# Kernel tuning notes

Hardware: AMD Instinct MI355X
Metric: run time of the kernel (lower is better)

The kernel has to match this reference:

```python
import jax, jax.numpy as jnp
import numpy as np

N_EMBD = 1024
N_FF = 4 * N_EMBD
N_EXPERTS = 8
TOP_K = 2
B, S = 1, 2048


def setup_inputs() -> dict:
    key = jax.random.key(0)
    ks = jax.random.split(key, 8)
    std = 0.02
    x = jax.random.normal(ks[0], (B, S, N_EMBD), dtype=jnp.float32)
    Wr = jax.random.normal(ks[1], (N_EMBD, N_EXPERTS), dtype=jnp.float32) * std
    br = jnp.zeros((N_EXPERTS,), dtype=jnp.float32)
    W1 = jax.random.normal(ks[2], (N_EXPERTS, N_EMBD, N_FF), dtype=jnp.float32) * std
    b1 = jnp.zeros((N_EXPERTS, N_FF), dtype=jnp.float32)
    W2 = jax.random.normal(ks[3], (N_EXPERTS, N_FF, N_EMBD), dtype=jnp.float32) * std
    b2 = jnp.zeros((N_EXPERTS, N_EMBD), dtype=jnp.float32)
    return {"x": x, "Wr": Wr, "br": br, "W1": W1, "b1": b1, "W2": W2, "b2": b2}


def reference(x, Wr, br, W1, b1, W2, b2):
    # x: [B, S, D]
    Bx, Sx, D = x.shape
    T = Bx * Sx
    E = Wr.shape[1]
    flat = x.reshape(T, D)

    # Router: softmax over experts, top-k, renormalize top-k weights
    logits = flat @ Wr + br                      # [T, E]
    probs = jax.nn.softmax(logits, axis=-1)
    topk_w, topk_i = jax.lax.top_k(probs, TOP_K)  # [T, K]
    topk_w = topk_w / jnp.sum(topk_w, axis=-1, keepdims=True)

    # Per-token combined expert weights (0 for non-selected experts).
    # Equivalent to the original gather/index_add combine.
    tok = jnp.arange(T)[:, None]
    w = jnp.zeros((T, E), dtype=flat.dtype).at[tok, topk_i].add(topk_w)  # [T, E]

    # Dense grouped expert MLP (exact GELU, matching torch nn.GELU default).
    h = jnp.einsum('td,edh->teh', flat, W1) + b1          # [T, E, 4D]
    h = jax.nn.gelu(h, approximate=False)
    y = jnp.einsum('teh,ehd->ted', h, W2) + b2            # [T, E, D]

    out = jnp.einsum('ted,te->td', y, w)                  # weighted combine
    return out.reshape(Bx, Sx, D)
```

## Files before the change

kernel.cpp:

```cpp
#include <hip/hip_runtime.h>
#include <stdint.h>

#define T_TOK 2048
#define DIM   1024
#define HID   4096
#define NEXP  8

typedef __attribute__((ext_vector_type(8))) short  short8;
typedef __attribute__((ext_vector_type(4))) short  short4v;
typedef __attribute__((ext_vector_type(4))) float  floatx4;
typedef __attribute__((ext_vector_type(4))) int    intx4;

__device__ __forceinline__ ushort f2bf(float f) {
    union { float f; uint32_t i; } v; v.f = f;
    uint32_t r = v.i + 0x7FFFu + ((v.i >> 16) & 1u);
    return (ushort)(r >> 16);
}
__device__ __forceinline__ float gelu_exact(float x) {
    return 0.5f * x * (1.0f + erff(x * 0.70710678118654752f));
}
__device__ __forceinline__ void glds16(const ushort* g, ushort* lds) {
    __builtin_amdgcn_global_load_lds(
        (const __attribute__((address_space(1))) unsigned int*)g,
        (__attribute__((address_space(3))) unsigned int*)lds, 16, 0, 0);
}

__global__ __launch_bounds__(256) void cast_x_kernel(
    const float* __restrict__ x, ushort* __restrict__ Xb)
{
    int i = (blockIdx.x * 256 + threadIdx.x) * 8;
    floatx4 a = *(const floatx4*)(x + i);
    floatx4 b = *(const floatx4*)(x + i + 4);
    uint32_t o[4];
    o[0] = (uint32_t)f2bf(a[0]) | ((uint32_t)f2bf(a[1]) << 16);
    o[1] = (uint32_t)f2bf(a[2]) | ((uint32_t)f2bf(a[3]) << 16);
    o[2] = (uint32_t)f2bf(b[0]) | ((uint32_t)f2bf(b[1]) << 16);
    o[3] = (uint32_t)f2bf(b[2]) | ((uint32_t)f2bf(b[3]) << 16);
    *(intx4*)(Xb + i) = *(const intx4*)o;
}

__global__ __launch_bounds__(256) void transpose_cast_kernel(
    const float* __restrict__ in, ushort* __restrict__ out, int R, int C)
{
    __shared__ float tile[64][65];
    int e = blockIdx.z;
    int rb = blockIdx.y * 64, cb = blockIdx.x * 64;
    const float* ip = in + (size_t)e * R * C;
    ushort* op = out + (size_t)e * R * C;
    int t = threadIdx.x;
    int tr = t >> 4, tc4 = (t & 15) * 4;
#pragma unroll
    for (int i = 0; i < 4; i++) {
        int r = i * 16 + tr;
        floatx4 v = *(const floatx4*)(ip + (size_t)(rb + r) * C + cb + tc4);
        tile[r][tc4] = v[0]; tile[r][tc4 + 1] = v[1];
        tile[r][tc4 + 2] = v[2]; tile[r][tc4 + 3] = v[3];
    }
    __syncthreads();
    int cc = t >> 2, rseg = (t & 3) * 16;
#pragma unroll
    for (int s = 0; s < 2; s++) {
        ushort o[8];
#pragma unroll
        for (int j = 0; j < 8; j++) o[j] = f2bf(tile[rseg + s * 8 + j][cc]);
        *(intx4*)(op + (size_t)(cb + cc) * R + rb + rseg + s * 8) = *(const intx4*)o;
    }
}

__global__ __launch_bounds__(256) void router_kernel(
    const float* __restrict__ x, const float* __restrict__ Wr,
    const float* __restrict__ br, int* __restrict__ counts,
    int* __restrict__ tlist, float* __restrict__ wlist)
{
    int wv = threadIdx.x >> 6, l = threadIdx.x & 63;
    int t = blockIdx.x * 4 + wv;
    float acc[NEXP];
#pragma unroll
    for (int e = 0; e < NEXP; e++) acc[e] = 0.f;
    const float* xr = x + (size_t)t * DIM;
    for (int d = l; d < DIM; d += 64) {
        float xv = xr[d];
        floatx4 w0 = *(const floatx4*)(Wr + (size_t)d * NEXP);
        floatx4 w1 = *(const floatx4*)(Wr + (size_t)d * NEXP + 4);
#pragma unroll
        for (int e = 0; e < 4; e++) { acc[e] += xv * w0[e]; acc[e + 4] += xv * w1[e]; }
    }
#pragma unroll
    for (int e = 0; e < NEXP; e++) {
#pragma unroll
        for (int off = 32; off; off >>= 1) acc[e] += __shfl_xor(acc[e], off, 64);
    }
    if (l == 0) {
        float lg[NEXP];
#pragma unroll
        for (int e = 0; e < NEXP; e++) lg[e] = acc[e] + br[e];
        int e0 = 0;
#pragma unroll
        for (int e = 1; e < NEXP; e++) if (lg[e] > lg[e0]) e0 = e;
        int e1 = -1;
#pragma unroll
        for (int e = 0; e < NEXP; e++) {
            if (e == e0) continue;
            if (e1 < 0 || lg[e] > lg[e1]) e1 = e;
        }
        float w0 = 1.f / (1.f + expf(lg[e1] - lg[e0]));
        float w1 = 1.f - w0;
        int s0 = atomicAdd(&counts[e0], 1);
        tlist[e0 * T_TOK + s0] = t;
        wlist[e0 * T_TOK + s0] = w0;
        int s1 = atomicAdd(&counts[e1], 1);
        tlist[e1 * T_TOK + s1] = t | (1 << 16);
        wlist[e1 * T_TOK + s1] = w1;
    }
}

template <int MODE>
__global__ __launch_bounds__(256, 2) void moe_gemm2(
    const ushort* __restrict__ A, const ushort* __restrict__ Wt,
    const float* __restrict__ bias, const int* __restrict__ counts,
    const int* __restrict__ tlist, const float* __restrict__ wlist,
    ushort* __restrict__ Hout, float* __restrict__ Yout)
{
    constexpr int NTOT  = MODE ? DIM : HID;
    constexpr int KFULL = MODE ? HID : DIM;
    constexpr int KLEN  = MODE ? 2048 : 1024;

    int bx = blockIdx.x;
    int e, mt, nt, kc;
    if (MODE == 0) { e = bx >> 9; mt = (bx >> 5) & 15; nt = bx & 31; kc = 0; }
    else { e = bx >> 8; int rr = bx & 255; mt = rr >> 4; nt = (rr >> 1) & 7; kc = rr & 1; }

    int Ne = counts[e];
    if (mt * 128 >= Ne) return;

    __shared__ ushort ldsA[4096];
    __shared__ ushort ldsB[4096];

    int tid = threadIdx.x, wv = tid >> 6, l = tid & 63;
    int srow = (wv & 1) * 64 + l;
    int kq = (wv >> 1) * 8;

    int slot = mt * 128 + srow; if (slot >= Ne) slot = Ne - 1;
    int packed = tlist[e * T_TOK + slot];
    int tok = packed & 0xFFFF, rk = (packed >> 16) & 1;
    size_t arow = MODE ? (size_t)(tok * 2 + rk) : (size_t)tok;
    const ushort* aptr = A + arow * KFULL + kc * 2048 + kq;
    const ushort* bptr = Wt + (size_t)e * NTOT * KFULL
                            + (size_t)(nt * 128 + srow) * KFULL + kc * 2048 + kq;

    ushort* la0 = &ldsA[wv * 512];
    ushort* la1 = &ldsA[2048 + wv * 512];
    ushort* lb0 = &ldsB[wv * 512];
    ushort* lb1 = &ldsB[2048 + wv * 512];

    int wm = wv >> 1, wn = wv & 1, q = l >> 4, lr = l & 15;
    int aoff[4], boff[4];
#pragma unroll
    for (int mi = 0; mi < 4; mi++) aoff[mi] = q * 1024 + (wm * 64 + mi * 16 + lr) * 8;
#pragma unroll
    for (int ni = 0; ni < 4; ni++) boff[ni] = q * 1024 + (wn * 64 + ni * 16 + lr) * 8;

    floatx4 zz = {0.f, 0.f, 0.f, 0.f};
    floatx4 acc[4][4];
#pragma unroll
    for (int mi = 0; mi < 4; mi++)
#pragma unroll
        for (int ni = 0; ni < 4; ni++) acc[mi][ni] = zz;

    for (int k0 = 0; k0 < KLEN; k0 += 32) {
        __syncthreads();
        glds16(aptr + k0,      la0);
        glds16(aptr + k0 + 16, la1);
        glds16(bptr + k0,      lb0);
        glds16(bptr + k0 + 16, lb1);
        __syncthreads();

        short8 af[4], bfv[4];
#pragma unroll
        for (int mi = 0; mi < 4; mi++) af[mi] = *(const short8*)&ldsA[aoff[mi]];
#pragma unroll
        for (int ni = 0; ni < 4; ni++) bfv[ni] = *(const short8*)&ldsB[boff[ni]];
#pragma unroll
        for (int mi = 0; mi < 4; mi++)
#pragma unroll
            for (int ni = 0; ni < 4; ni++)
                acc[mi][ni] = __builtin_amdgcn_mfma_f32_16x16x32_bf16(
                    af[mi], bfv[ni], acc[mi][ni], 0, 0, 0);
    }

#pragma unroll
    for (int mi = 0; mi < 4; mi++) {
        int rbase = wm * 64 + mi * 16 + q * 4;
#pragma unroll
        for (int j = 0; j < 4; j++) {
            int slot2 = mt * 128 + rbase + j;
            if (slot2 >= Ne) continue;
            int pk2 = tlist[e * T_TOK + slot2];
            int tok2 = pk2 & 0xFFFF, rk2 = (pk2 >> 16) & 1;
#pragma unroll
            for (int ni = 0; ni < 4; ni++) {
                int col = nt * 128 + wn * 64 + ni * 16 + lr;
                float v = acc[mi][ni][j];
                float bc = bias[e * NTOT + col];
                if (MODE == 0) {
                    v = gelu_exact(v + bc);
                    Hout[(size_t)(tok2 * 2 + rk2) * HID + col] = f2bf(v);
                } else {
                    if (kc == 0) v += bc;
                    v *= wlist[e * T_TOK + slot2];
                    atomicAdd(&Yout[(size_t)tok2 * DIM + col], v);
                }
            }
        }
    }
}

template <int MODE>
__global__ __launch_bounds__(256, 2) void moe_gemm(
    const ushort* __restrict__ A, const float* __restrict__ W,
    const float* __restrict__ bias, const int* __restrict__ counts,
    const int* __restrict__ tlist, const float* __restrict__ wlist,
    ushort* __restrict__ Hout, float* __restrict__ Yacc)
{
    constexpr int NTOT = MODE ? DIM : HID;
    constexpr int AROW = MODE ? HID : DIM;
    constexpr int KLEN = MODE ? 2048 : 1024;

    int bx = blockIdx.x;
    int e, mt, nt, kc;
    if (MODE == 0) { e = bx >> 9; mt = (bx >> 5) & 15; nt = bx & 31; kc = 0; }
    else { e = bx >> 8; int r = bx & 255; mt = r >> 4; nt = (r >> 1) & 7; kc = r & 1; }

    int Ne = counts[e];
    if (mt * 128 >= Ne) return;

    size_t wbase = (size_t)e * DIM * HID + (size_t)kc * 2048 * NTOT + (size_t)nt * 128;

    __shared__ ushort ldsA[128 * 40];
    __shared__ ushort ldsB[128 * 36];

    int tid = threadIdx.x;
    int wv = tid >> 6, l = tid & 63;

    const ushort* arowp[2]; int apos[2];
#pragma unroll
    for (int i = 0; i < 2; i++) {
        int idx = i * 256 + tid;
        int r = idx >> 2, p = idx & 3;
        int slot = mt * 128 + r; if (slot >= Ne) slot = Ne - 1;
        int packed = tlist[e * T_TOK + slot];
        int tok = packed & 0xFFFF, rk = (packed >> 16) & 1;
        size_t arow = MODE ? (size_t)(tok * 2 + rk) : (size_t)tok;
        arowp[i] = A + arow * AROW + (MODE ? kc * 2048 : 0) + p * 8;
        apos[i] = r * 40 + p * 8;
    }

    int kp = tid & 15;
    int n8 = tid >> 4;
    size_t boffg = wbase + (size_t)(2 * kp) * NTOT + n8 * 8;

    int wm = wv >> 1, wn = wv & 1;
    int q = l >> 4;
    int aoff[4], boff[4];
#pragma unroll
    for (int mi = 0; mi < 4; mi++)
        aoff[mi] = (wm * 64 + mi * 16 + (l & 15)) * 40 + q * 8;
#pragma unroll
    for (int ni = 0; ni < 4; ni++)
        boff[ni] = (wn * 64 + ni * 16 + (l & 15)) * 36 + q * 8;

    floatx4 zz = {0.f, 0.f, 0.f, 0.f};
    floatx4 acc[4][4];
#pragma unroll
    for (int mi = 0; mi < 4; mi++)
#pragma unroll
        for (int ni = 0; ni < 4; ni++) acc[mi][ni] = zz;

    for (int k0 = 0; k0 < KLEN; k0 += 32) {
        intx4 av[2];
#pragma unroll
        for (int i = 0; i < 2; i++) av[i] = *(const intx4*)(arowp[i] + k0);
        const float* p0 = W + boffg + (size_t)k0 * NTOT;
        const float* p1 = p0 + NTOT;
        floatx4 a0 = *(const floatx4*)(p0);
        floatx4 a1 = *(const floatx4*)(p0 + 4);
        floatx4 b0 = *(const floatx4*)(p1);
        floatx4 b1 = *(const floatx4*)(p1 + 4);
        uint32_t pr[8];
#pragma unroll
        for (int j = 0; j < 8; j++) {
            float va = (j < 4) ? a0[j & 3] : a1[j & 3];
            float vb = (j < 4) ? b0[j & 3] : b1[j & 3];
            pr[j] = (uint32_t)f2bf(va) | ((uint32_t)f2bf(vb) << 16);
        }

        __syncthreads();
#pragma unroll
        for (int i = 0; i < 2; i++) *(intx4*)&ldsA[apos[i]] = av[i];
#pragma unroll
        for (int j = 0; j < 8; j++)
            *(uint32_t*)&ldsB[(n8 * 8 + j) * 36 + 2 * kp] = pr[j];
        __syncthreads();

        short8 af[4], bf[4];
#pragma unroll
        for (int mi = 0; mi < 4; mi++) af[mi] = *(const short8*)&ldsA[aoff[mi]];
#pragma unroll
        for (int ni = 0; ni < 4; ni++) {
            short4v blo = *(const short4v*)&ldsB[boff[ni]];
            short4v bhi = *(const short4v*)&ldsB[boff[ni] + 4];
            bf[ni] = __builtin_shufflevector(blo, bhi, 0, 1, 2, 3, 4, 5, 6, 7);
        }
#pragma unroll
        for (int mi = 0; mi < 4; mi++)
#pragma unroll
            for (int ni = 0; ni < 4; ni++)
                acc[mi][ni] = __builtin_amdgcn_mfma_f32_16x16x32_bf16(
                    af[mi], bf[ni], acc[mi][ni], 0, 0, 0);
    }

#pragma unroll
    for (int mi = 0; mi < 4; mi++) {
        int rbase = wm * 64 + mi * 16 + q * 4;
#pragma unroll
        for (int j = 0; j < 4; j++) {
            int slot = mt * 128 + rbase + j;
            if (slot >= Ne) continue;
            int packed = tlist[e * T_TOK + slot];
            int tok = packed & 0xFFFF, rk = (packed >> 16) & 1;
#pragma unroll
            for (int ni = 0; ni < 4; ni++) {
                int col = nt * 128 + wn * 64 + ni * 16 + (l & 15);
                float v = acc[mi][ni][j];
                float bc = bias[e * NTOT + col];
                if (MODE == 0) {
                    v = gelu_exact(v + bc);
                    Hout[(size_t)(tok * 2 + rk) * HID + col] = f2bf(v);
                } else {
                    if (kc == 0) v += bc;
                    v *= wlist[e * T_TOK + slot];
                    atomicAdd(&Yacc[(size_t)tok * DIM + col], v);
                }
            }
        }
    }
}

__global__ __launch_bounds__(256) void combine_kernel(
    const float* __restrict__ Y, float* __restrict__ out)
{
    int i = (blockIdx.x * 256 + threadIdx.x) * 4;
    *(floatx4*)(out + i) = *(const floatx4*)(Y + i);
}

extern "C" void kernel_launch(void* const* d_in, const int* in_sizes, int n_in,
                              void* d_out, int out_size, void* d_ws, size_t ws_size,
                              hipStream_t stream) {
    const float* x  = (const float*)d_in[0];
    const float* Wr = (const float*)d_in[1];
    const float* br = (const float*)d_in[2];
    const float* W1 = (const float*)d_in[3];
    const float* b1 = (const float*)d_in[4];
    const float* W2 = (const float*)d_in[5];
    const float* b2 = (const float*)d_in[6];
    float* out = (float*)d_out;
    char* ws = (char*)d_ws;

    if (ws_size >= 104988928ULL) {
        int*    counts = (int*)ws;
        int*    tlist  = (int*)(ws + 256);
        float*  wlist  = (float*)(ws + 65792);
        ushort* Xb     = (ushort*)(ws + 131328);
        ushort* Hbuf   = (ushort*)(ws + 4325632);
        ushort* Wt     = (ushort*)(ws + 37880064);

        hipMemsetAsync(counts, 0, 256, stream);
        hipMemsetAsync(out, 0, (size_t)T_TOK * DIM * sizeof(float), stream);
        cast_x_kernel<<<T_TOK * DIM / 2048, 256, 0, stream>>>(x, Xb);
        router_kernel<<<T_TOK / 4, 256, 0, stream>>>(x, Wr, br, counts, tlist, wlist);
        transpose_cast_kernel<<<dim3(HID / 64, DIM / 64, NEXP), 256, 0, stream>>>(
            W1, Wt, DIM, HID);
        moe_gemm2<0><<<NEXP * 16 * 32, 256, 0, stream>>>(
            Xb, Wt, b1, counts, tlist, wlist, Hbuf, nullptr);
        transpose_cast_kernel<<<dim3(DIM / 64, HID / 64, NEXP), 256, 0, stream>>>(
            W2, Wt, HID, DIM);
        moe_gemm2<1><<<NEXP * 16 * 8 * 2, 256, 0, stream>>>(
            Hbuf, Wt, b2, counts, tlist, wlist, nullptr, out);
    } else {
        int*    counts = (int*)ws;
        int*    tlist  = (int*)(ws + 256);
        float*  wlist  = (float*)(ws + 256 + 65536);
        ushort* Hbuf   = (ushort*)(ws + 256 + 131072);
        float*  Yacc   = (float*)(ws + 256 + 131072 + 33554432);
        ushort* Xb     = (ushort*)Yacc;

        hipMemsetAsync(counts, 0, 256, stream);
        cast_x_kernel<<<T_TOK * DIM / 2048, 256, 0, stream>>>(x, Xb);
        router_kernel<<<T_TOK / 4, 256, 0, stream>>>(x, Wr, br, counts, tlist, wlist);
        moe_gemm<0><<<NEXP * 16 * 32, 256, 0, stream>>>(Xb, W1, b1, counts, tlist, wlist, Hbuf, nullptr);
        hipMemsetAsync(Yacc, 0, (size_t)T_TOK * DIM * sizeof(float), stream);
        moe_gemm<1><<<NEXP * 16 * 8 * 2, 256, 0, stream>>>(Hbuf, W2, b2, counts, tlist, wlist, nullptr, Yacc);
        combine_kernel<<<out_size / 1024, 256, 0, stream>>>(Yacc, out);
    }
}
```

Measured before the change: 656.9 us.

## Double-buffer LDS tiles with K=64 stages in grouped MoE GEMM

Replaces the single-buffered K=32 global-to-LDS loop with a double-buffered K=64 pipeline: the next tile is issued via global_load_lds before computing on the current one, using explicit vmcnt waits and barriers. Each stage now runs two MFMA k-substeps, halving barrier count per K and hiding global load latency behind compute. LDS grows to 64KB per block, which may limit occupancy to the launch-bound target of 2 blocks per CU and relies on hand-written waitcnt correctness.

```diff
diff --git a/kernel.cpp b/kernel.cpp
--- a/kernel.cpp
+++ b/kernel.cpp
@@ -115,7 +115,7 @@
 }
 
 template <int MODE>
-__global__ __launch_bounds__(256, 2) void moe_gemm2(
+__global__ __launch_bounds__(256, 2) void moe_gemm3(
     const ushort* __restrict__ A, const ushort* __restrict__ Wt,
     const float* __restrict__ bias, const int* __restrict__ counts,
     const int* __restrict__ tlist, const float* __restrict__ wlist,
@@ -124,6 +124,7 @@
     constexpr int NTOT  = MODE ? DIM : HID;
     constexpr int KFULL = MODE ? HID : DIM;
     constexpr int KLEN  = MODE ? 2048 : 1024;
+    constexpr int NTILE = KLEN / 64;
 
     int bx = blockIdx.x;
     int e, mt, nt, kc;
@@ -133,32 +134,41 @@
     int Ne = counts[e];
     if (mt * 128 >= Ne) return;
 
-    __shared__ ushort ldsA[4096];
-    __shared__ ushort ldsB[4096];
+    __shared__ ushort lds[32768];
 
     int tid = threadIdx.x, wv = tid >> 6, l = tid & 63;
-    int srow = (wv & 1) * 64 + l;
-    int kq = (wv >> 1) * 8;
-
-    int slot = mt * 128 + srow; if (slot >= Ne) slot = Ne - 1;
-    int packed = tlist[e * T_TOK + slot];
-    int tok = packed & 0xFFFF, rk = (packed >> 16) & 1;
-    size_t arow = MODE ? (size_t)(tok * 2 + rk) : (size_t)tok;
-    const ushort* aptr = A + arow * KFULL + kc * 2048 + kq;
-    const ushort* bptr = Wt + (size_t)e * NTOT * KFULL
-                            + (size_t)(nt * 128 + srow) * KFULL + kc * 2048 + kq;
-
-    ushort* la0 = &ldsA[wv * 512];
-    ushort* la1 = &ldsA[2048 + wv * 512];
-    ushort* lb0 = &ldsB[wv * 512];
-    ushort* lb1 = &ldsB[2048 + wv * 512];
-
-    int wm = wv >> 1, wn = wv & 1, q = l >> 4, lr = l & 15;
-    int aoff[4], boff[4];
-#pragma unroll
-    for (int mi = 0; mi < 4; mi++) aoff[mi] = q * 1024 + (wm * 64 + mi * 16 + lr) * 8;
-#pragma unroll
-    for (int ni = 0; ni < 4; ni++) boff[ni] = q * 1024 + (wn * 64 + ni * 16 + lr) * 8;
+
+    int s0 = mt * 128 + l;      if (s0 >= Ne) s0 = Ne - 1;
+    int s1 = mt * 128 + 64 + l; if (s1 >= Ne) s1 = Ne - 1;
+    int p0 = tlist[e * T_TOK + s0], p1 = tlist[e * T_TOK + s1];
+    size_t ar0 = MODE ? (size_t)((p0 & 0xFFFF) * 2 + ((p0 >> 16) & 1)) : (size_t)(p0 & 0xFFFF);
+    size_t ar1 = MODE ? (size_t)((p1 & 0xFFFF) * 2 + ((p1 >> 16) & 1)) : (size_t)(p1 & 0xFFFF);
+    const ushort* asrc0 = A + ar0 * KFULL + kc * 2048;
+    const ushort* asrc1 = A + ar1 * KFULL + kc * 2048;
+    const ushort* bsrc0 = Wt + (size_t)e * NTOT * KFULL
+                             + (size_t)(nt * 128 + l) * KFULL + kc * 2048;
+    const ushort* bsrc1 = bsrc0 + (size_t)64 * KFULL;
+    int q0 = wv, q1 = wv + 4;
+
+#define STAGE(buf, t) do {                                             \
+        ushort* Lb = &lds[(buf) * 16384];                              \
+        int ko = (t) * 64;                                             \
+        glds16(asrc0 + ko + q0 * 8, Lb + q0 * 1024);                   \
+        glds16(asrc0 + ko + q1 * 8, Lb + q1 * 1024);                   \
+        glds16(asrc1 + ko + q0 * 8, Lb + q0 * 1024 + 512);             \
+        glds16(asrc1 + ko + q1 * 8, Lb + q1 * 1024 + 512);             \
+        glds16(bsrc0 + ko + q0 * 8, Lb + 8192 + q0 * 1024);            \
+        glds16(bsrc0 + ko + q1 * 8, Lb + 8192 + q1 * 1024);            \
+        glds16(bsrc1 + ko + q0 * 8, Lb + 8192 + q0 * 1024 + 512);      \
+        glds16(bsrc1 + ko + q1 * 8, Lb + 8192 + q1 * 1024 + 512);      \
+    } while (0)
+
+    int wm = wv >> 1, wn = wv & 1, q4 = l >> 4, lr = l & 15;
+    int aro[4], bro[4];
+#pragma unroll
+    for (int mi = 0; mi < 4; mi++) aro[mi] = (wm * 64 + mi * 16 + lr) * 8;
+#pragma unroll
+    for (int ni = 0; ni < 4; ni++) bro[ni] = 8192 + (wn * 64 + ni * 16 + lr) * 8;
 
     floatx4 zz = {0.f, 0.f, 0.f, 0.f};
     floatx4 acc[4][4];
@@ -167,30 +177,44 @@
 #pragma unroll
         for (int ni = 0; ni < 4; ni++) acc[mi][ni] = zz;
 
-    for (int k0 = 0; k0 < KLEN; k0 += 32) {
-        __syncthreads();
-        glds16(aptr + k0,      la0);
-        glds16(aptr + k0 + 16, la1);
-        glds16(bptr + k0,      lb0);
-        glds16(bptr + k0 + 16, lb1);
-        __syncthreads();
-
+    STAGE(0, 0);
+    int cur = 0;
+    for (int t = 0; t < NTILE; ++t) {
+        asm volatile("" ::: "memory");
+        __builtin_amdgcn_s_barrier();
+        asm volatile("" ::: "memory");
+        if (t + 1 < NTILE) {
+            STAGE(cur ^ 1, t + 1);
+            asm volatile("s_waitcnt vmcnt(8)" ::: "memory");
+        } else {
+            asm volatile("s_waitcnt vmcnt(0)" ::: "memory");
+        }
+        __builtin_amdgcn_s_barrier();
+        asm volatile("" ::: "memory");
+
+        const ushort* Lp = &lds[cur * 16384];
         short8 af[4], bfv[4];
 #pragma unroll
-        for (int mi = 0; mi < 4; mi++) af[mi] = *(const short8*)&ldsA[aoff[mi]];
-#pragma unroll
-        for (int ni = 0; ni < 4; ni++) bfv[ni] = *(const short8*)&ldsB[boff[ni]];
-#pragma unroll
-        for (int mi = 0; mi < 4; mi++)
-#pragma unroll
-            for (int ni = 0; ni < 4; ni++)
-                acc[mi][ni] = __builtin_amdgcn_mfma_f32_16x16x32_bf16(
-                    af[mi], bfv[ni], acc[mi][ni], 0, 0, 0);
-    }
+        for (int kk = 0; kk < 2; ++kk) {
+            int qb = (kk * 4 + q4) * 1024;
+#pragma unroll
+            for (int ni = 0; ni < 4; ni++) bfv[ni] = *(const short8*)&Lp[qb + bro[ni]];
+#pragma unroll
+            for (int mi = 0; mi < 4; mi++) af[mi] = *(const short8*)&Lp[qb + aro[mi]];
+#pragma unroll
+            for (int mi = 0; mi < 4; mi++)
+#pragma unroll
+                for (int ni = 0; ni < 4; ni++)
+                    acc[mi][ni] = __builtin_amdgcn_mfma_f32_16x16x32_bf16(
+                        af[mi], bfv[ni], acc[mi][ni], 0, 0, 0);
+        }
+        cur ^= 1;
+    }
+#undef STAGE
 
 #pragma unroll
     for (int mi = 0; mi < 4; mi++) {
-        int rbase = wm * 64 + mi * 16 + q * 4;
+        int rbase = wm * 64 + mi * 16 + q4 * 4;
 #pragma unroll
         for (int j = 0; j < 4; j++) {
             int slot2 = mt * 128 + rbase + j;
@@ -380,11 +404,11 @@
         router_kernel<<<T_TOK / 4, 256, 0, stream>>>(x, Wr, br, counts, tlist, wlist);
         transpose_cast_kernel<<<dim3(HID / 64, DIM / 64, NEXP), 256, 0, stream>>>(
             W1, Wt, DIM, HID);
-        moe_gemm2<0><<<NEXP * 16 * 32, 256, 0, stream>>>(
+        moe_gemm3<0><<<NEXP * 16 * 32, 256, 0, stream>>>(
             Xb, Wt, b1, counts, tlist, wlist, Hbuf, nullptr);
         transpose_cast_kernel<<<dim3(DIM / 64, HID / 64, NEXP), 256, 0, stream>>>(
             W2, Wt, HID, DIM);
-        moe_gemm2<1><<<NEXP * 16 * 8 * 2, 256, 0, stream>>>(
+        moe_gemm3<1><<<NEXP * 16 * 8 * 2, 256, 0, stream>>>(
             Hbuf, Wt, b2, counts, tlist, wlist, nullptr, out);
     } else {
         int*    counts = (int*)ws;
```

New measurement: 607.1 us. -7.6%, faster.
